# Performance work log

Hardware: AMD Instinct MI355X
Metric: run time of the kernel (lower is better)

Reference implementation:

```python
import jax, jax.numpy as jnp
import numpy as np

B, T, E, H = 8, 2048, 1024, 128

def setup_inputs() -> dict:
    key = jax.random.key(0)
    kx, kq, kk, kv = jax.random.split(key, 4)
    x = jax.random.normal(kx, (B, T, E), dtype=jnp.float32)
    # Linear(E, H, bias=False) weights, stored as (E, H) so y = x @ W
    s = 1.0 / np.sqrt(E)
    Wq = jax.random.normal(kq, (E, H), dtype=jnp.float32) * s
    Wk = jax.random.normal(kk, (E, H), dtype=jnp.float32) * s
    Wv = jax.random.normal(kv, (E, H), dtype=jnp.float32) * s
    return {"x": x, "Wq": Wq, "Wk": Wk, "Wv": Wv}

def reference(x, Wq, Wk, Wv):
    # x: (B, T, E)
    Tcur = x.shape[1]
    q = jnp.einsum('bte,eh->bth', x, Wq)
    k = jnp.einsum('bte,eh->bth', x, Wk)
    v = jnp.einsum('bte,eh->bth', x, Wv)
    scores = jnp.einsum('bqh,bkh->bqk', q, k)  # (B, T, T)
    # NOTE: source multiplies by x.shape[2]**0.5 where x.shape[2] == T here
    scores = scores * jnp.sqrt(jnp.asarray(Tcur, dtype=scores.dtype))
    causal = jnp.tril(jnp.ones((Tcur, Tcur), dtype=bool))
    scores = jnp.where(causal, scores, -jnp.inf)
    attn = jax.nn.softmax(scores, axis=2)
    # dropout p=0.0 -> identity
    return jnp.einsum('bqk,bkh->bqh', attn, v)
```

## Files before the change

kernel.cpp:

```cpp
#include <hip/hip_runtime.h>
#include <hip/hip_bf16.h>
#include <math.h>

#define B_ 8
#define T_ 2048
#define E_ 1024
#define H_ 128
#define M_ (B_*T_)
#define SCALE_ 45.25483399593904f
#define SEG_ 4

typedef __attribute__((ext_vector_type(8))) short bf16x8;
typedef __attribute__((ext_vector_type(4))) float f32x4;

#define mfma16(A, Bv, C) __builtin_amdgcn_mfma_f32_16x16x32_bf16((A), (Bv), (C), 0, 0, 0)

#define FRAGW(g, kc, lane)  ((((size_t)(g)*32 + (kc))*64 + (lane))*8)
#define FRAGK(b, kt16, kc, lane) (((((size_t)(b)*128 + (kt16))*4 + (kc))*64 + (lane))*8)
#define FRAGV(b, ht, kt32, lane) (((((size_t)(b)*8 + (ht))*64 + (kt32))*64 + (lane))*8)

__device__ __forceinline__ ushort bf16_rne(float f) {
  unsigned u = __float_as_uint(f);
  u += 0x7fffu + ((u >> 16) & 1u);
  return (ushort)(u >> 16);
}
__device__ __forceinline__ float bf16_tof(ushort h) {
  return __uint_as_float(((unsigned)h) << 16);
}

template <int N>
__device__ __forceinline__ float ror16(float x) {
  return __uint_as_float((unsigned)__builtin_amdgcn_update_dpp(
      0, (int)__float_as_uint(x), 0x120 + N, 0xF, 0xF, true));
}
__device__ __forceinline__ float rowmax16(float x) {
  x = fmaxf(x, ror16<8>(x));
  x = fmaxf(x, ror16<4>(x));
  x = fmaxf(x, ror16<2>(x));
  x = fmaxf(x, ror16<1>(x));
  return x;
}
__device__ __forceinline__ float rowsum16(float x) {
  x += ror16<8>(x);
  x += ror16<4>(x);
  x += ror16<2>(x);
  x += ror16<1>(x);
  return x;
}

__global__ __launch_bounds__(256) void wsplit(
    const float* __restrict__ Wq, const float* __restrict__ Wk,
    const float* __restrict__ Wv,
    ushort* __restrict__ whT, ushort* __restrict__ wlT)
{
  const int idx  = blockIdx.x * 256 + threadIdx.x;
  const int mat  = idx >> 14;
  const int rem  = idx & 16383;
  const int nt   = rem >> 11;
  const int kc   = (rem >> 6) & 31;
  const int lane = rem & 63;
  const int quad = lane >> 4, l15 = lane & 15;
  const float* W = (mat == 0) ? Wq : (mat == 1) ? Wk : Wv;
  const int n  = nt * 16 + l15;
  const int k0 = kc * 32 + quad * 8;
  bf16x8 hv, lv;
  #pragma unroll
  for (int j = 0; j < 8; ++j) {
    const float f = W[(size_t)(k0 + j) * H_ + n];
    const ushort h = bf16_rne(f);
    hv[j] = (short)h;
    lv[j] = (short)bf16_rne(f - bf16_tof(h));
  }
  *(bf16x8*)(whT + (size_t)idx * 8) = hv;
  *(bf16x8*)(wlT + (size_t)idx * 8) = lv;
}

#define PSTEP(KC, BH, BL, BHN, BLN) do {                                      \
    __syncthreads();                                                          \
    {                                                                         \
      const float f_[8] = {xf0.x, xf0.y, xf0.z, xf0.w,                        \
                           xf1.x, xf1.y, xf1.z, xf1.w};                       \
      bf16x8 hv_, lv_;                                                        \
      _Pragma("unroll")                                                       \
      for (int jj_ = 0; jj_ < 8; ++jj_) {                                     \
        const ushort h_ = bf16_rne(f_[jj_]);                                  \
        hv_[jj_] = (short)h_;                                                 \
        lv_[jj_] = (short)bf16_rne(f_[jj_] - bf16_tof(h_));                   \
      }                                                                       \
      *(bf16x8*)&AhS[ca * 8] = hv_;                                           \
      *(bf16x8*)&AlS[ca * 8] = lv_;                                           \
    }                                                                         \
    __syncthreads();                                                          \
    if ((KC) + 1 < 32) {                                                      \
      const float* s_ = x + (size_t)(m0 + arow) * E_ + ((KC) + 1) * 32 + akoff;\
      xf0 = *(const float4*)s_;                                               \
      xf1 = *(const float4*)(s_ + 4);                                         \
      _Pragma("unroll")                                                       \
      for (int j_ = 0; j_ < 3; ++j_) {                                        \
        const int g_ = g0 + 4 * j_;                                           \
        BHN[j_] = *(const bf16x8*)(whT + FRAGW(g_, (KC) + 1, lane));          \
        if (g_ < 16)                                                          \
          BLN[j_] = *(const bf16x8*)(wlT + FRAGW(g_, (KC) + 1, lane));        \
      }                                                                       \
    }                                                                         \
    bf16x8 a_h_[4], a_l_[4];                                                  \
    _Pragma("unroll")                                                         \
    for (int mt_ = 0; mt_ < 4; ++mt_) {                                       \
      a_h_[mt_] = *(const bf16x8*)&AhS[(((mt_ * 4 + quad) * 16) + l15) * 8];  \
      a_l_[mt_] = *(const bf16x8*)&AlS[(((mt_ * 4 + quad) * 16) + l15) * 8];  \
    }                                                                         \
    _Pragma("unroll")                                                         \
    for (int j_ = 0; j_ < 3; ++j_) {                                          \
      const int g_ = g0 + 4 * j_;                                             \
      if (g_ < 16) {                                                          \
        _Pragma("unroll")                                                     \
        for (int mt_ = 0; mt_ < 4; ++mt_) {                                   \
          acc[j_][mt_] = mfma16(a_h_[mt_], BH[j_], acc[j_][mt_]);             \
          acc[j_][mt_] = mfma16(a_h_[mt_], BL[j_], acc[j_][mt_]);             \
          acc[j_][mt_] = mfma16(a_l_[mt_], BH[j_], acc[j_][mt_]);             \
        }                                                                     \
      } else {                                                                \
        _Pragma("unroll")                                                     \
        for (int mt_ = 0; mt_ < 4; ++mt_)                                     \
          acc[j_][mt_] = mfma16(a_h_[mt_], BH[j_], acc[j_][mt_]);             \
      }                                                                       \
    }                                                                         \
  } while (0)

__global__ __launch_bounds__(256) void proj_fused(
    const float* __restrict__ x,
    const ushort* __restrict__ whT, const ushort* __restrict__ wlT,
    ushort* __restrict__ qh, ushort* __restrict__ ql,
    ushort* __restrict__ kfh, ushort* __restrict__ kfl,
    ushort* __restrict__ vF)
{
  const int m0   = blockIdx.x * 64;
  const int half = blockIdx.y;
  const int tid  = threadIdx.x;
  const int wave = tid >> 6, lane = tid & 63;
  const int quad = lane >> 4, l15 = lane & 15;

  __shared__ __align__(16) ushort SM[9216];
  ushort* AhS = SM;
  ushort* AlS = SM + 2048;

  f32x4 acc[3][4];
  #pragma unroll
  for (int j = 0; j < 3; ++j)
    #pragma unroll
    for (int mt = 0; mt < 4; ++mt) acc[j][mt] = (f32x4){0.f, 0.f, 0.f, 0.f};

  const int arow  = tid >> 2;
  const int akoff = (tid & 3) * 8;
  const int ca    = ((arow >> 4) * 4 + (tid & 3)) * 16 + (arow & 15);
  const int g0    = half * 12 + wave;

  float4 xf0, xf1;
  bf16x8 bhA[3], blA[3], bhB[3], blB[3];
  {
    const float* s = x + (size_t)(m0 + arow) * E_ + akoff;
    xf0 = *(const float4*)s;
    xf1 = *(const float4*)(s + 4);
    #pragma unroll
    for (int j = 0; j < 3; ++j) {
      const int g = g0 + 4 * j;
      bhA[j] = *(const bf16x8*)(whT + FRAGW(g, 0, lane));
      if (g < 16) blA[j] = *(const bf16x8*)(wlT + FRAGW(g, 0, lane));
    }
  }

  int kc = 0;
  while (true) {
    PSTEP(kc, bhA, blA, bhB, blB); if (++kc == 32) break;
    PSTEP(kc, bhB, blB, bhA, blA); if (++kc == 32) break;
  }

  #pragma unroll
  for (int j = 0; j < 3; ++j) {
    const int g = g0 + 4 * j;
    if (g < 8) {
      const int ncol = g * 16 + l15;
      #pragma unroll
      for (int mt = 0; mt < 4; ++mt)
        #pragma unroll
        for (int r = 0; r < 4; ++r) {
          const float a = acc[j][mt][r];
          const ushort h = bf16_rne(a);
          const size_t off = (size_t)(m0 + mt * 16 + quad * 4 + r) * H_ + ncol;
          qh[off] = h;
          ql[off] = bf16_rne(a - bf16_tof(h));
        }
    } else if (g < 16) {
      const int hcol = (g - 8) * 16 + l15;
      const int kch  = hcol >> 5;
      const int qdh  = (hcol >> 3) & 3;
      const int jj   = hcol & 7;
      #pragma unroll
      for (int mt = 0; mt < 4; ++mt)
        #pragma unroll
        for (int r = 0; r < 4; ++r) {
          const float a = acc[j][mt][r];
          const int tg = m0 + mt * 16 + quad * 4 + r;
          const int bb = tg >> 11, tl = tg & 2047;
          const size_t ad = FRAGK(bb, tl >> 4, kch, qdh * 16 + (tl & 15)) + jj;
          const ushort h = bf16_rne(a);
          kfh[ad] = h;
          kfl[ad] = bf16_rne(a - bf16_tof(h));
        }
    }
  }
  if (half == 1) {
    __syncthreads();
    ushort* smT = SM;
    #pragma unroll
    for (int j = 1; j < 3; ++j) {
      const int g = 12 + wave + 4 * j;
      const int hcol = (g - 16) * 16 + l15;
      #pragma unroll
      for (int mt = 0; mt < 4; ++mt)
        #pragma unroll
        for (int r = 0; r < 4; ++r)
          smT[hcol * 72 + mt * 16 + quad * 4 + r] = bf16_rne(acc[j][mt][r]);
    }
    __syncthreads();
    const int bb = m0 >> 11, t0 = m0 & 2047;
    #pragma unroll
    for (int u = 0; u < 4; ++u) {
      const int c   = u * 256 + tid;
      const int ht  = c >> 7;
      const int ktl = (c >> 6) & 1;
      const int lv  = c & 63;
      const int qv  = lv >> 4, l15v = lv & 15;
      *(bf16x8*)(vF + FRAGV(bb, ht, (t0 >> 5) + ktl, lv)) =
          *(const bf16x8*)&smT[(ht * 16 + l15v) * 72 + ktl * 32 + qv * 8];
    }
  }
}

__global__ __launch_bounds__(256) void attn_flash(
    const ushort* __restrict__ qh, const ushort* __restrict__ ql,
    const ushort* __restrict__ kfh, const ushort* __restrict__ kfl,
    const ushort* __restrict__ vF,
    ushort* __restrict__ Opart, float* __restrict__ mlpart)
{
  const int b    = (int)blockIdx.x & 7;
  const int seg  = (int)blockIdx.x >> 3;
  const int qt   = 31 - (int)blockIdx.y;
  const int q0   = qt * 64;
  const int tid  = threadIdx.x;
  const int wave = tid >> 6, lane = tid & 63;
  const int quad = lane >> 4, l15 = lane & 15;
  const f32x4 z4 = (f32x4){0.f, 0.f, 0.f, 0.f};

  __shared__ __align__(16) ushort KhS[4096];
  __shared__ __align__(16) ushort KlS[4096];
  __shared__ __align__(16) ushort VtS[4096];
  __shared__ __align__(16) ushort smP[4 * 640];

  const int ntiles = 2 * qt + 2;
  const int cnt    = (ntiles + SEG_ - 1) >> 2;
  const int jt0    = seg * cnt;
  const int jt1    = (jt0 + cnt < ntiles) ? (jt0 + cnt) : ntiles;

  const int q0w = q0 + wave * 16;
  const int ntw = ((q0w + 15) >> 5) + 1;
  const size_t pidx = ((size_t)(b * 128 + qt * 4 + wave)) * SEG_ + seg;
  ushort* op = Opart + pidx * 2048;
  float*  ml = mlpart + pidx * 32;

  if (jt0 >= jt1) {
    const bf16x8 zz = {0, 0, 0, 0, 0, 0, 0, 0};
    #pragma unroll
    for (int u = 0; u < 4; ++u)
      *(bf16x8*)(op + lane * 32 + u * 8) = zz;
    if (lane < 32) ml[lane] = (lane & 1) ? 0.f : -1e30f;
    return;
  }

  const size_t base = (size_t)b * T_ * H_;

  const ushort* qhp = qh + base + (size_t)(q0w + l15) * H_ + quad * 8;
  const ushort* qlp = ql + base + (size_t)(q0w + l15) * H_ + quad * 8;
  bf16x8 Qh[4], Ql[4];
  #pragma unroll
  for (int c = 0; c < 4; ++c) {
    Qh[c] = *(const bf16x8*)(qhp + c * 32);
    Ql[c] = *(const bf16x8*)(qlp + c * 32);
  }

  f32x4 O[8];
  #pragma unroll
  for (int i = 0; i < 8; ++i) O[i] = z4;
  float mstate[4] = {-1e30f, -1e30f, -1e30f, -1e30f};
  float lstate[4] = {0.f, 0.f, 0.f, 0.f};

  bf16x8 rkh[2], rkl[2], rv[2];
  {
    #pragma unroll
    for (int u = 0; u < 2; ++u) {
      const int c = u * 256 + tid;
      rkh[u] = *(const bf16x8*)(kfh + FRAGK(b, 2 * jt0 + (c >> 8), (c >> 6) & 3, c & 63));
      rkl[u] = *(const bf16x8*)(kfl + FRAGK(b, 2 * jt0 + (c >> 8), (c >> 6) & 3, c & 63));
      rv[u]  = *(const bf16x8*)(vF  + FRAGV(b, c >> 6, jt0, c & 63));
    }
  }

  for (int jt = jt0; jt < jt1; ++jt) {
    __syncthreads();
    #pragma unroll
    for (int u = 0; u < 2; ++u) {
      const int c = u * 256 + tid;
      *(bf16x8*)&KhS[c * 8] = rkh[u];
      *(bf16x8*)&KlS[c * 8] = rkl[u];
      *(bf16x8*)&VtS[c * 8] = rv[u];
    }
    __syncthreads();

    if (jt + 1 < jt1) {
      #pragma unroll
      for (int u = 0; u < 2; ++u) {
        const int c = u * 256 + tid;
        rkh[u] = *(const bf16x8*)(kfh + FRAGK(b, 2 * (jt + 1) + (c >> 8), (c >> 6) & 3, c & 63));
        rkl[u] = *(const bf16x8*)(kfl + FRAGK(b, 2 * (jt + 1) + (c >> 8), (c >> 6) & 3, c & 63));
        rv[u]  = *(const bf16x8*)(vF  + FRAGV(b, c >> 6, jt + 1, c & 63));
      }
    }

    if (jt < ntw) {
      const int k0 = jt * 32;
      f32x4 shh0 = z4, shh1 = z4, sx0 = z4, sx1 = z4;
      #pragma unroll
      for (int c = 0; c < 4; ++c) {
        const bf16x8 kh0 = *(const bf16x8*)&KhS[(c * 64 + lane) * 8];
        const bf16x8 kh1 = *(const bf16x8*)&KhS[((4 + c) * 64 + lane) * 8];
        const bf16x8 kl0 = *(const bf16x8*)&KlS[(c * 64 + lane) * 8];
        const bf16x8 kl1 = *(const bf16x8*)&KlS[((4 + c) * 64 + lane) * 8];
        shh0 = mfma16(Qh[c], kh0, shh0);
        shh1 = mfma16(Qh[c], kh1, shh1);
        sx0  = mfma16(Qh[c], kl0, sx0);
        sx1  = mfma16(Qh[c], kl1, sx1);
        sx0  = mfma16(Ql[c], kh0, sx0);
        sx1  = mfma16(Ql[c], kh1, sx1);
      }

      float s0[4], s1[4];
      #pragma unroll
      for (int r = 0; r < 4; ++r) {
        s0[r] = (shh0[r] + sx0[r]) * SCALE_;
        s1[r] = (shh1[r] + sx1[r]) * SCALE_;
      }
      if (jt == ntw - 1) {
        const int krel0 = k0 + l15      - q0w - quad * 4;
        const int krel1 = k0 + 16 + l15 - q0w - quad * 4;
        #pragma unroll
        for (int r = 0; r < 4; ++r) {
          if (krel0 > r) s0[r] = -1e30f;
          if (krel1 > r) s1[r] = -1e30f;
        }
      }

      float alpha[4];
      #pragma unroll
      for (int r = 0; r < 4; ++r) {
        const float rm   = rowmax16(fmaxf(s0[r], s1[r]));
        const float mnew = fmaxf(mstate[r], rm);
        alpha[r] = __expf(mstate[r] - mnew);
        mstate[r] = mnew;
        const float p0 = __expf(s0[r] - mnew);
        const float p1 = __expf(s1[r] - mnew);
        lstate[r] = lstate[r] * alpha[r] + rowsum16(p0 + p1);
        smP[wave * 640 + (quad * 4 + r) * 40 + l15]      = bf16_rne(p0);
        smP[wave * 640 + (quad * 4 + r) * 40 + 16 + l15] = bf16_rne(p1);
      }
      #pragma unroll
      for (int ct = 0; ct < 8; ++ct) {
        O[ct][0] *= alpha[0]; O[ct][1] *= alpha[1];
        O[ct][2] *= alpha[2]; O[ct][3] *= alpha[3];
      }
      const bf16x8 pA = *(const bf16x8*)&smP[wave * 640 + l15 * 40 + quad * 8];
      #pragma unroll
      for (int ct = 0; ct < 8; ++ct) {
        const bf16x8 vf = *(const bf16x8*)&VtS[(ct * 64 + lane) * 8];
        O[ct] = mfma16(pA, vf, O[ct]);
      }
    }
  }

  #pragma unroll
  for (int r = 0; r < 4; ++r)
    #pragma unroll
    for (int ct = 0; ct < 8; ++ct)
      op[(quad * 4 + r) * 128 + ct * 16 + l15] = bf16_rne(O[ct][r]);
  if (l15 == 0) {
    #pragma unroll
    for (int r = 0; r < 4; ++r) {
      ml[(quad * 4 + r) * 2]     = mstate[r];
      ml[(quad * 4 + r) * 2 + 1] = lstate[r];
    }
  }
}

__global__ __launch_bounds__(256) void attn_combine(
    const ushort* __restrict__ Opart, const float* __restrict__ mlpart,
    float* __restrict__ out)
{
  const int idx = blockIdx.x * 256 + threadIdx.x;
  const int c4  = idx & 31;
  const int r   = idx >> 5;
  const int t   = r & 2047;
  const int qt  = t >> 4, r16 = t & 15;
  const size_t pb = ((size_t)((r >> 11) * 128 + qt)) * SEG_;

  float m[SEG_], l[SEG_];
  #pragma unroll
  for (int s = 0; s < SEG_; ++s) {
    m[s] = mlpart[(pb + s) * 32 + r16 * 2];
    l[s] = mlpart[(pb + s) * 32 + r16 * 2 + 1];
  }
  float M = m[0];
  #pragma unroll
  for (int s = 1; s < SEG_; ++s) M = fmaxf(M, m[s]);
  float w[SEG_], L = 0.f;
  #pragma unroll
  for (int s = 0; s < SEG_; ++s) {
    w[s] = __expf(m[s] - M);
    L += l[s] * w[s];
  }
  float4 acc = make_float4(0.f, 0.f, 0.f, 0.f);
  #pragma unroll
  for (int s = 0; s < SEG_; ++s) {
    const ushort4 o = *(const ushort4*)(Opart + (pb + s) * 2048 + r16 * 128 + c4 * 4);
    acc.x += w[s] * bf16_tof(o.x);
    acc.y += w[s] * bf16_tof(o.y);
    acc.z += w[s] * bf16_tof(o.z);
    acc.w += w[s] * bf16_tof(o.w);
  }
  const float inv = 1.0f / L;
  *(float4*)(out + (size_t)r * H_ + c4 * 4) =
      make_float4(acc.x * inv, acc.y * inv, acc.z * inv, acc.w * inv);
}

extern "C" void kernel_launch(void* const* d_in, const int* in_sizes, int n_in,
                              void* d_out, int out_size, void* d_ws, size_t ws_size,
                              hipStream_t stream) {
  (void)in_sizes; (void)n_in; (void)out_size; (void)ws_size;
  const float* x  = (const float*)d_in[0];
  const float* Wq = (const float*)d_in[1];
  const float* Wk = (const float*)d_in[2];
  const float* Wv = (const float*)d_in[3];
  float* out = (float*)d_out;

  ushort* qhb = (ushort*)d_ws;
  ushort* qlb = qhb + (size_t)M_ * H_;
  ushort* kfh = qlb + (size_t)M_ * H_;
  ushort* kfl = kfh + (size_t)M_ * H_;
  ushort* vFb = kfl + (size_t)M_ * H_;
  ushort* whT = vFb + (size_t)M_ * H_;
  ushort* wlT = whT + (size_t)3 * H_ * E_;
  ushort* Opart = wlT + (size_t)3 * H_ * E_;
  float*  mlpart = (float*)(Opart + (size_t)B_ * 128 * SEG_ * 2048);

  wsplit<<<dim3(192), 256, 0, stream>>>(Wq, Wk, Wv, whT, wlT);
  proj_fused<<<dim3(M_/64, 2), 256, 0, stream>>>(x, whT, wlT,
                                                 qhb, qlb, kfh, kfl, vFb);
  attn_flash<<<dim3(B_*SEG_, 32), 256, 0, stream>>>(qhb, qlb, kfh, kfl, vFb,
                                                    Opart, mlpart);
  attn_combine<<<dim3(2048), 256, 0, stream>>>(Opart, mlpart, out);
}
```

Baseline: 185.5 us.

## Double-buffer LDS in projection GEMM and balance Q/K/V work across halves

The projection kernel now double-buffers the split-bf16 x tile in LDS, so each k-step needs one barrier instead of two, and the global loads for the next tile are issued before the MFMAs run. Column groups are redistributed so each half computes 8 Q-or-K groups plus 4 V groups. Every wave therefore does the same 3-pass/1-pass MFMA mix, and both halves write their share of V. This removes the load imbalance and the barrier stalls, at the cost of a deeper register prefetch of x.

```diff
diff --git a/kernel.cpp b/kernel.cpp
--- a/kernel.cpp
+++ b/kernel.cpp
@@ -26,6 +26,11 @@
 }
 __device__ __forceinline__ float bf16_tof(ushort h) {
   return __uint_as_float(((unsigned)h) << 16);
+}
+
+__device__ __forceinline__ void lds_barrier() {
+  asm volatile("s_waitcnt lgkmcnt(0)" ::: "memory");
+  __builtin_amdgcn_s_barrier();
 }
 
 template <int N>
@@ -75,9 +80,26 @@
   *(bf16x8*)(wlT + (size_t)idx * 8) = lv;
 }
 
-#define PSTEP(KC, BH, BL, BHN, BLN) do {                                      \
-    __syncthreads();                                                          \
-    {                                                                         \
+#define PSTEP2(KC, CUR, NXT, BHC, BLC, BHN, BLN) do {                         \
+    bf16x8 a_h_[4], a_l_[4];                                                  \
+    _Pragma("unroll")                                                         \
+    for (int mt_ = 0; mt_ < 4; ++mt_) {                                       \
+      a_h_[mt_] = *(const bf16x8*)                                            \
+          &SM[(CUR)*4096 + (((mt_*4 + quad)*16) + l15)*8];                    \
+      a_l_[mt_] = *(const bf16x8*)                                            \
+          &SM[(CUR)*4096 + 2048 + (((mt_*4 + quad)*16) + l15)*8];             \
+    }                                                                         \
+    float4 nf0_, nf1_;                                                        \
+    if ((KC) + 2 < 32) {                                                      \
+      nf0_ = *(const float4*)(xrow + ((KC) + 2)*32);                          \
+      nf1_ = *(const float4*)(xrow + ((KC) + 2)*32 + 4);                      \
+    } else { nf0_ = xf0; nf1_ = xf1; }                                        \
+    if ((KC) + 1 < 32) {                                                      \
+      BHN[0] = *(const bf16x8*)(whT + FRAGW(gq,     (KC)+1, lane));           \
+      BHN[1] = *(const bf16x8*)(whT + FRAGW(gq + 4, (KC)+1, lane));           \
+      BHN[2] = *(const bf16x8*)(whT + FRAGW(gv,     (KC)+1, lane));           \
+      BLN[0] = *(const bf16x8*)(wlT + FRAGW(gq,     (KC)+1, lane));           \
+      BLN[1] = *(const bf16x8*)(wlT + FRAGW(gq + 4, (KC)+1, lane));           \
       const float f_[8] = {xf0.x, xf0.y, xf0.z, xf0.w,                        \
                            xf1.x, xf1.y, xf1.z, xf1.w};                       \
       bf16x8 hv_, lv_;                                                        \
@@ -87,44 +109,21 @@
         hv_[jj_] = (short)h_;                                                 \
         lv_[jj_] = (short)bf16_rne(f_[jj_] - bf16_tof(h_));                   \
       }                                                                       \
-      *(bf16x8*)&AhS[ca * 8] = hv_;                                           \
-      *(bf16x8*)&AlS[ca * 8] = lv_;                                           \
+      *(bf16x8*)&SM[(NXT)*4096 + ca*8] = hv_;                                 \
+      *(bf16x8*)&SM[(NXT)*4096 + 2048 + ca*8] = lv_;                          \
     }                                                                         \
-    __syncthreads();                                                          \
-    if ((KC) + 1 < 32) {                                                      \
-      const float* s_ = x + (size_t)(m0 + arow) * E_ + ((KC) + 1) * 32 + akoff;\
-      xf0 = *(const float4*)s_;                                               \
-      xf1 = *(const float4*)(s_ + 4);                                         \
-      _Pragma("unroll")                                                       \
-      for (int j_ = 0; j_ < 3; ++j_) {                                        \
-        const int g_ = g0 + 4 * j_;                                           \
-        BHN[j_] = *(const bf16x8*)(whT + FRAGW(g_, (KC) + 1, lane));          \
-        if (g_ < 16)                                                          \
-          BLN[j_] = *(const bf16x8*)(wlT + FRAGW(g_, (KC) + 1, lane));        \
-      }                                                                       \
-    }                                                                         \
-    bf16x8 a_h_[4], a_l_[4];                                                  \
     _Pragma("unroll")                                                         \
     for (int mt_ = 0; mt_ < 4; ++mt_) {                                       \
-      a_h_[mt_] = *(const bf16x8*)&AhS[(((mt_ * 4 + quad) * 16) + l15) * 8];  \
-      a_l_[mt_] = *(const bf16x8*)&AlS[(((mt_ * 4 + quad) * 16) + l15) * 8];  \
+      acc[0][mt_] = mfma16(a_h_[mt_], BHC[0], acc[0][mt_]);                   \
+      acc[0][mt_] = mfma16(a_h_[mt_], BLC[0], acc[0][mt_]);                   \
+      acc[0][mt_] = mfma16(a_l_[mt_], BHC[0], acc[0][mt_]);                   \
+      acc[1][mt_] = mfma16(a_h_[mt_], BHC[1], acc[1][mt_]);                   \
+      acc[1][mt_] = mfma16(a_h_[mt_], BLC[1], acc[1][mt_]);                   \
+      acc[1][mt_] = mfma16(a_l_[mt_], BHC[1], acc[1][mt_]);                   \
+      acc[2][mt_] = mfma16(a_h_[mt_], BHC[2], acc[2][mt_]);                   \
     }                                                                         \
-    _Pragma("unroll")                                                         \
-    for (int j_ = 0; j_ < 3; ++j_) {                                          \
-      const int g_ = g0 + 4 * j_;                                             \
-      if (g_ < 16) {                                                          \
-        _Pragma("unroll")                                                     \
-        for (int mt_ = 0; mt_ < 4; ++mt_) {                                   \
-          acc[j_][mt_] = mfma16(a_h_[mt_], BH[j_], acc[j_][mt_]);             \
-          acc[j_][mt_] = mfma16(a_h_[mt_], BL[j_], acc[j_][mt_]);             \
-          acc[j_][mt_] = mfma16(a_l_[mt_], BH[j_], acc[j_][mt_]);             \
-        }                                                                     \
-      } else {                                                                \
-        _Pragma("unroll")                                                     \
-        for (int mt_ = 0; mt_ < 4; ++mt_)                                     \
-          acc[j_][mt_] = mfma16(a_h_[mt_], BH[j_], acc[j_][mt_]);             \
-      }                                                                       \
-    }                                                                         \
+    xf0 = nf0_; xf1 = nf1_;                                                   \
+    lds_barrier();                                                            \
   } while (0)
 
 __global__ __launch_bounds__(256) void proj_fused(
@@ -140,9 +139,7 @@
   const int wave = tid >> 6, lane = tid & 63;
   const int quad = lane >> 4, l15 = lane & 15;
 
-  __shared__ __align__(16) ushort SM[9216];
-  ushort* AhS = SM;
-  ushort* AlS = SM + 2048;
+  __shared__ __align__(16) ushort SM[8192];
 
   f32x4 acc[3][4];
   #pragma unroll
@@ -153,32 +150,47 @@
   const int arow  = tid >> 2;
   const int akoff = (tid & 3) * 8;
   const int ca    = ((arow >> 4) * 4 + (tid & 3)) * 16 + (arow & 15);
-  const int g0    = half * 12 + wave;
+  const int gq    = half * 8 + wave;
+  const int gv    = 16 + half * 4 + wave;
+
+  const float* xrow = x + (size_t)(m0 + arow) * E_ + akoff;
 
   float4 xf0, xf1;
-  bf16x8 bhA[3], blA[3], bhB[3], blB[3];
+  bf16x8 bhA[3], blA[2], bhB[3], blB[2];
+
   {
-    const float* s = x + (size_t)(m0 + arow) * E_ + akoff;
-    xf0 = *(const float4*)s;
-    xf1 = *(const float4*)(s + 4);
-    #pragma unroll
-    for (int j = 0; j < 3; ++j) {
-      const int g = g0 + 4 * j;
-      bhA[j] = *(const bf16x8*)(whT + FRAGW(g, 0, lane));
-      if (g < 16) blA[j] = *(const bf16x8*)(wlT + FRAGW(g, 0, lane));
-    }
-  }
+    const float4 f0 = *(const float4*)xrow;
+    const float4 f1 = *(const float4*)(xrow + 4);
+    const float f_[8] = {f0.x, f0.y, f0.z, f0.w, f1.x, f1.y, f1.z, f1.w};
+    bf16x8 hv, lv;
+    #pragma unroll
+    for (int jj = 0; jj < 8; ++jj) {
+      const ushort h = bf16_rne(f_[jj]);
+      hv[jj] = (short)h;
+      lv[jj] = (short)bf16_rne(f_[jj] - bf16_tof(h));
+    }
+    *(bf16x8*)&SM[ca * 8] = hv;
+    *(bf16x8*)&SM[2048 + ca * 8] = lv;
+    xf0 = *(const float4*)(xrow + 32);
+    xf1 = *(const float4*)(xrow + 36);
+    bhA[0] = *(const bf16x8*)(whT + FRAGW(gq,     0, lane));
+    bhA[1] = *(const bf16x8*)(whT + FRAGW(gq + 4, 0, lane));
+    bhA[2] = *(const bf16x8*)(whT + FRAGW(gv,     0, lane));
+    blA[0] = *(const bf16x8*)(wlT + FRAGW(gq,     0, lane));
+    blA[1] = *(const bf16x8*)(wlT + FRAGW(gq + 4, 0, lane));
+  }
+  lds_barrier();
 
   int kc = 0;
   while (true) {
-    PSTEP(kc, bhA, blA, bhB, blB); if (++kc == 32) break;
-    PSTEP(kc, bhB, blB, bhA, blA); if (++kc == 32) break;
-  }
-
-  #pragma unroll
-  for (int j = 0; j < 3; ++j) {
-    const int g = g0 + 4 * j;
-    if (g < 8) {
+    PSTEP2(kc, 0, 1, bhA, blA, bhB, blB); if (++kc == 32) break;
+    PSTEP2(kc, 1, 0, bhB, blB, bhA, blA); if (++kc == 32) break;
+  }
+
+  #pragma unroll
+  for (int j = 0; j < 2; ++j) {
+    const int g = gq + 4 * j;
+    if (half == 0) {
       const int ncol = g * 16 + l15;
       #pragma unroll
       for (int mt = 0; mt < 4; ++mt)
@@ -190,7 +202,7 @@
           qh[off] = h;
           ql[off] = bf16_rne(a - bf16_tof(h));
         }
-    } else if (g < 16) {
+    } else {
       const int hcol = (g - 8) * 16 + l15;
       const int kch  = hcol >> 5;
       const int qdh  = (hcol >> 3) & 3;
@@ -209,30 +221,26 @@
         }
     }
   }
-  if (half == 1) {
-    __syncthreads();
+  __syncthreads();
+  {
     ushort* smT = SM;
-    #pragma unroll
-    for (int j = 1; j < 3; ++j) {
-      const int g = 12 + wave + 4 * j;
-      const int hcol = (g - 16) * 16 + l15;
-      #pragma unroll
-      for (int mt = 0; mt < 4; ++mt)
-        #pragma unroll
-        for (int r = 0; r < 4; ++r)
-          smT[hcol * 72 + mt * 16 + quad * 4 + r] = bf16_rne(acc[j][mt][r]);
-    }
+    const int lh = wave * 16 + l15;
+    #pragma unroll
+    for (int mt = 0; mt < 4; ++mt)
+      #pragma unroll
+      for (int r = 0; r < 4; ++r)
+        smT[lh * 72 + mt * 16 + quad * 4 + r] = bf16_rne(acc[2][mt][r]);
     __syncthreads();
     const int bb = m0 >> 11, t0 = m0 & 2047;
     #pragma unroll
-    for (int u = 0; u < 4; ++u) {
-      const int c   = u * 256 + tid;
-      const int ht  = c >> 7;
-      const int ktl = (c >> 6) & 1;
-      const int lv  = c & 63;
-      const int qv  = lv >> 4, l15v = lv & 15;
-      *(bf16x8*)(vF + FRAGV(bb, ht, (t0 >> 5) + ktl, lv)) =
-          *(const bf16x8*)&smT[(ht * 16 + l15v) * 72 + ktl * 32 + qv * 8];
+    for (int u = 0; u < 2; ++u) {
+      const int c    = u * 256 + tid;
+      const int lht  = c >> 7;
+      const int ktl  = (c >> 6) & 1;
+      const int lv   = c & 63;
+      const int qv   = lv >> 4, l15v = lv & 15;
+      *(bf16x8*)(vF + FRAGV(bb, half * 4 + lht, (t0 >> 5) + ktl, lv)) =
+          *(const bf16x8*)&smT[(lht * 16 + l15v) * 72 + ktl * 32 + qv * 8];
     }
   }
 }
```

Measured after the change: 177.7 us. -4.2%, faster.
